# Kernel tuning notes

Hardware: AMD Instinct MI355X
Metric: run time of the kernel (lower is better)

## Reference

```python
import jax, jax.numpy as jnp
import numpy as np

N_TV_ITER = 20      # fixed Chambolle iteration count (skimage early-stops via eps; fixed for jit)
TV_WEIGHT = 0.1


def _div(p):
    # negative adjoint of forward-difference gradient (skimage convention)
    d = -(p[0] + p[1])
    d = d.at[1:, :].add(p[0, :-1, :])
    d = d.at[:, 1:].add(p[1, :, :-1])
    return d


def tv_chambolle_2d(image):
    """skimage.restoration.denoise_tv_chambolle on a single 2D image, weight=0.1."""
    tau = 0.25  # 1 / (2 * ndim)

    def step(p, _):
        out = image + _div(p)
        gy = jnp.zeros_like(out).at[:-1, :].set(out[1:, :] - out[:-1, :])
        gx = jnp.zeros_like(out).at[:, :-1].set(out[:, 1:] - out[:, :-1])
        norm = jnp.sqrt(gy * gy + gx * gx)
        g = jnp.stack([gy, gx])
        p = (p - tau * g) / (1.0 + (tau / TV_WEIGHT) * norm)
        return p, None

    p0 = jnp.zeros((2,) + image.shape, image.dtype)
    p, _ = jax.lax.scan(step, p0, None, length=N_TV_ITER)
    return image + _div(p)


def tv_denoise(img):  # [B,C,H,W], vmapped over B*C (replaces the CPU python loop)
    B, C, H, W = img.shape
    out = jax.vmap(tv_chambolle_2d)(img.reshape(B * C, H, W))
    return out.reshape(B, C, H, W)


def conv(x, w, stride=1, groups=1):
    pad = w.shape[2] // 2  # 'same'-style padding for odd kernels, 0 for 1x1
    return jax.lax.conv_general_dilated(
        x, w, (stride, stride), [(pad, pad), (pad, pad)],
        dimension_numbers=('NCHW', 'OIHW', 'NCHW'),
        feature_group_count=groups)


def haar_ll(x):
    # one level of pywt wavedec2('haar') LL band: 0.5 * sum over each 2x2 block
    return 0.5 * (x[..., ::2, ::2] + x[..., ::2, 1::2] + x[..., 1::2, ::2] + x[..., 1::2, 1::2])


def backbone(x, stem_w, dw_pw):
    # stride-32, 1280-channel EfficientNet-B0-style feature extractor
    x = jax.nn.silu(conv(x, stem_w, stride=2))
    for dw, pw in dw_pw:
        x = jax.nn.silu(conv(x, dw, stride=2, groups=dw.shape[0]))
        x = jax.nn.silu(conv(x, pw))
    return x


def setup_inputs() -> dict:
    key = jax.random.key(0)
    ks = jax.random.split(key, 16)
    B, H, W = 4, 512, 512

    def w(k, o, i, kh, kw):
        return jax.random.normal(k, (o, i, kh, kw), jnp.float32) * (1.0 / np.sqrt(i * kh * kw))

    return {
        "img": jax.random.normal(ks[0], (B, 1, H, W), jnp.float32),
        "stem_w": w(ks[1], 32, 1, 3, 3),
        "dw1_w": w(ks[2], 32, 1, 3, 3),  "pw1_w": w(ks[3], 64, 32, 1, 1),
        "dw2_w": w(ks[4], 64, 1, 3, 3),  "pw2_w": w(ks[5], 128, 64, 1, 1),
        "dw3_w": w(ks[6], 128, 1, 3, 3), "pw3_w": w(ks[7], 256, 128, 1, 1),
        "dw4_w": w(ks[8], 256, 1, 3, 3), "pw4_w": w(ks[9], 512, 256, 1, 1),
        "head_w": w(ks[10], 1280, 512, 1, 1),
        "proj_w": w(ks[11], 64, 1280, 1, 1),
        "proj_b": jnp.zeros((64,), jnp.float32),
        "final_w": w(ks[12], 1, 64, 1, 1),
        "final_b": jnp.zeros((1,), jnp.float32),
    }


def reference(img, stem_w, dw1_w, pw1_w, dw2_w, pw2_w, dw3_w, pw3_w, dw4_w, pw4_w,
              head_w, proj_w, proj_b, final_w, final_b):
    B, C, H, W = img.shape
    x = tv_denoise(img)                                     # fused TV Chambolle
    x = backbone(x, stem_w, [(dw1_w, pw1_w), (dw2_w, pw2_w), (dw3_w, pw3_w), (dw4_w, pw4_w)])
    x = jax.nn.silu(conv(x, head_w))                        # [B,1280,H/32,W/32]
    x = conv(x, proj_w) + proj_b[None, :, None, None]       # [B,64,H/32,W/32]
    x = jax.image.resize(x, (B, 64, H, W), method='bilinear')  # align_corners=False semantics
    ll = haar_ll(haar_ll(x))                                # 2-level Haar LL: [B,64,H/4,W/4]
    out = conv(ll, final_w) + final_b[None, :, None, None]  # [B,1,H/4,W/4]
    return out
```

## Files before the change

### kernel.cpp

```cpp
#include <hip/hip_runtime.h>
#include <math.h>

constexpr int BATCH = 4;
constexpr int IMG_H = 512, IMG_W = 512;
constexpr int IMG_HW = IMG_H * IMG_W;
constexpr int PSTR = BATCH * IMG_HW;

constexpr size_t O_PA   = 0;
constexpr size_t O_PB   = O_PA + 2 * (size_t)PSTR;
constexpr size_t O_DEN  = O_PB + 2 * (size_t)PSTR;
constexpr size_t O_A1   = O_DEN + (size_t)PSTR;
constexpr size_t O_A2   = O_A1 + 8388608;
constexpr size_t O_WT1  = O_A2 + 2097152;
constexpr size_t O_WT2  = O_WT1 + 32 * 64;
constexpr size_t O_WT3  = O_WT2 + 64 * 128;
constexpr size_t O_WT4  = O_WT3 + 128 * 256;
constexpr size_t O_WTH  = O_WT4 + 256 * 512;
constexpr size_t O_WCOMB= O_WTH + 512 * 1280;
constexpr size_t O_BCOMB= O_WCOMB + 1280;
constexpr size_t O_S    = O_BCOMB + 4;
constexpr size_t WS_FLOATS = O_S + 1024;

__device__ __forceinline__ float fast_rcp(float x) { return __builtin_amdgcn_rcpf(x); }
__device__ __forceinline__ float fast_sqrt(float x) { return __builtin_amdgcn_sqrtf(x); }
__device__ __forceinline__ float silu_f(float x) {
    float e = __builtin_amdgcn_exp2f(-1.44269504088896f * x);
    return x * fast_rcp(1.0f + e);
}
__device__ __forceinline__ int clampi(int v, int lo, int hi) {
    return v < lo ? lo : (v > hi ? hi : v);
}

template <int NST, bool FIRST, bool LAST>
__global__ __launch_bounds__(512, 8) void tv_reg(const float* __restrict__ img,
                                                 const float* __restrict__ pin,
                                                 float* __restrict__ pout,
                                                 const float* __restrict__ pw1,
                                                 const float* __restrict__ pw2,
                                                 const float* __restrict__ pw3,
                                                 const float* __restrict__ pw4,
                                                 const float* __restrict__ headw,
                                                 const float* __restrict__ projw,
                                                 const float* __restrict__ projb,
                                                 const float* __restrict__ finalw,
                                                 float* __restrict__ ws) {
    constexpr int ROWS = 6, NW = 8, HL = 10, TC = 44, TR = 28;
    constexpr int TVY = 19;
    __shared__ float bndP[2][512], bndO[2][512];

    if constexpr (FIRST) {
        if (blockIdx.y >= TVY) {
            __shared__ float tt[32][33];
            const int tid = threadIdx.x;
            const int pid = ((blockIdx.y - TVY) * 4 + blockIdx.z) * 12 + blockIdx.x;
            for (int t = pid; t < 814; t += 96) {
                const float* src = nullptr; float* dst = nullptr;
                int C = 0, R = 0, tr = 0, tc = 0;
                if (t < 640) {
                    src = headw; dst = ws + O_WTH; R = 1280; C = 512; tr = t >> 4; tc = t & 15;
                } else if (t < 768) {
                    int e = t - 640; src = pw4; dst = ws + O_WT4; R = 512; C = 256; tr = e >> 3; tc = e & 7;
                } else if (t < 800) {
                    int e = t - 768; src = pw3; dst = ws + O_WT3; R = 256; C = 128; tr = e >> 2; tc = e & 3;
                } else if (t < 808) {
                    int e = t - 800; src = pw2; dst = ws + O_WT2; R = 128; C = 64; tr = e >> 1; tc = e & 1;
                } else if (t < 810) {
                    int e = t - 808; src = pw1; dst = ws + O_WT1; R = 64; C = 32; tr = e; tc = 0;
                }
                const int tx = tid & 31, ty = tid >> 5;
                __syncthreads();
                if (src) {
#pragma unroll
                    for (int j = 0; j < 2; ++j)
                        tt[ty + j * 16][tx] =
                            src[(size_t)(tr * 32 + ty + j * 16) * C + tc * 32 + tx];
                }
                __syncthreads();
                if (src) {
#pragma unroll
                    for (int j = 0; j < 2; ++j)
                        dst[(size_t)(tc * 32 + ty + j * 16) * R + tr * 32 + tx] =
                            tt[tx][ty + j * 16];
                } else if (t < 813) {
                    int k = (t - 810) * 512 + tid;
                    if (k < 1280) {
                        float a = 0.0f;
                        for (int ch = 0; ch < 64; ++ch)
                            a = fmaf(finalw[ch], projw[ch * 1280 + k], a);
                        ws[O_WCOMB + k] = a;
                    }
                } else {
                    if (tid == 0) {
                        float a = 0.0f;
                        for (int ch = 0; ch < 64; ++ch) a = fmaf(finalw[ch], projb[ch], a);
                        ws[O_BCOMB] = a;
                    }
                }
            }
            return;
        }
    }

    const int tid = threadIdx.x;
    const int lane = tid & 63, w = tid >> 6;
    const int b = blockIdx.z;
    const int r0 = blockIdx.y * TR, c0 = blockIdx.x * TC;
    const int gj = c0 - HL + lane;
    const int gjc = clampi(gj, 0, 511);
    const int gib = r0 - HL + w * ROWS;
    const float* I = img + b * IMG_HW;
    const bool interior = (r0 - HL >= 1) && (r0 + NW * ROWS - HL <= 511) &&
                          (c0 - HL >= 1) && (c0 + 64 - HL <= 511);

    float rim[ROWS], rp0[ROWS], rp1[ROWS], ro[ROWS];
#pragma unroll
    for (int k = 0; k < ROWS; ++k) {
        int gi = clampi(gib + k, 0, 511);
        rim[k] = I[(gi << 9) + gjc];
    }
    if (!FIRST) {
        const float* P0 = pin + b * IMG_HW;
        const float* P1 = pin + PSTR + b * IMG_HW;
#pragma unroll
        for (int k = 0; k < ROWS; ++k) {
            int gi = clampi(gib + k, 0, 511);
            rp0[k] = P0[(gi << 9) + gjc];
            rp1[k] = P1[(gi << 9) + gjc];
        }
    }
    const bool gjpos = (gj > 0), gjlt = (gj < 511);

    int s0 = 0;
    if (FIRST) {
        bndO[0][tid] = rim[0];
        __syncthreads();
        float odn = (w < NW - 1) ? bndO[0][tid + 64] : 0.0f;
        if (interior) {
#pragma unroll
            for (int k = 0; k < ROWS; ++k) {
                float oR = __shfl_down(rim[k], 1);
                float od = (k < ROWS - 1) ? rim[k + 1] : odn;
                float gy = od - rim[k];
                float gx = oR - rim[k];
                float inv = fast_rcp(fmaf(2.5f, fast_sqrt(fmaf(gy, gy, gx * gx)), 1.0f));
                rp0[k] = -0.25f * gy * inv;
                rp1[k] = -0.25f * gx * inv;
            }
        } else {
#pragma unroll
            for (int k = 0; k < ROWS; ++k) {
                float oR = __shfl_down(rim[k], 1);
                float od = (k < ROWS - 1) ? rim[k + 1] : odn;
                int gi = gib + k;
                float gy = (gi < 511) ? od - rim[k] : 0.0f;
                float gx = gjlt ? oR - rim[k] : 0.0f;
                float inv = fast_rcp(fmaf(2.5f, fast_sqrt(fmaf(gy, gy, gx * gx)), 1.0f));
                rp0[k] = -0.25f * gy * inv;
                rp1[k] = -0.25f * gx * inv;
            }
        }
        s0 = 1;
    }

    for (int s = s0; s < NST; ++s) {
        const int par = s & 1;
        float p1l0 = __shfl_up(rp1[0], 1);
        float partO = rim[0] - rp0[0] - rp1[0];
        if (interior) partO += p1l0;
        else if (gjpos) partO += p1l0;
        bndP[par][tid] = rp0[ROWS - 1];
        bndO[par][tid] = partO;
        __syncthreads();
        float pup0 = (w > 0) ? bndP[par][tid - 64] : 0.0f;
        float odn = (w < NW - 1) ? bndO[par][tid + 64] + rp0[ROWS - 1] : 0.0f;
        if (interior) {
            ro[0] = partO + pup0;
#pragma unroll
            for (int k = 1; k < ROWS; ++k) {
                float p1l = __shfl_up(rp1[k], 1);
                ro[k] = rim[k] - rp0[k] - rp1[k] + rp0[k - 1] + p1l;
            }
#pragma unroll
            for (int k = 0; k < ROWS; ++k) {
                float oR = __shfl_down(ro[k], 1);
                float od = (k < ROWS - 1) ? ro[k + 1] : odn;
                float gy = od - ro[k];
                float gx = oR - ro[k];
                float inv = fast_rcp(fmaf(2.5f, fast_sqrt(fmaf(gy, gy, gx * gx)), 1.0f));
                rp0[k] = (rp0[k] - 0.25f * gy) * inv;
                rp1[k] = (rp1[k] - 0.25f * gx) * inv;
            }
        } else {
            ro[0] = partO + ((gib > 0) ? pup0 : 0.0f);
#pragma unroll
            for (int k = 1; k < ROWS; ++k) {
                float p1l = __shfl_up(rp1[k], 1);
                float o = rim[k] - rp0[k] - rp1[k];
                if (gib + k > 0) o += rp0[k - 1];
                if (gjpos) o += p1l;
                ro[k] = o;
            }
#pragma unroll
            for (int k = 0; k < ROWS; ++k) {
                float oR = __shfl_down(ro[k], 1);
                float od = (k < ROWS - 1) ? ro[k + 1] : odn;
                int gi = gib + k;
                float gy = (gi < 511) ? od - ro[k] : 0.0f;
                float gx = gjlt ? oR - ro[k] : 0.0f;
                float inv = fast_rcp(fmaf(2.5f, fast_sqrt(fmaf(gy, gy, gx * gx)), 1.0f));
                rp0[k] = (rp0[k] - 0.25f * gy) * inv;
                rp1[k] = (rp1[k] - 0.25f * gx) * inv;
            }
        }
    }

    const bool cst = (lane >= HL && lane < HL + TC && gj < 512);
    if (LAST) {
        constexpr int epar = NST & 1;
        bndP[epar][tid] = rp0[ROWS - 1];
        __syncthreads();
        float pup0 = (w > 0) ? bndP[epar][tid - 64] : 0.0f;
        float* D = pout + b * IMG_HW;
#pragma unroll
        for (int k = 0; k < ROWS; ++k) {
            float p1l = __shfl_up(rp1[k], 1);
            int gi = gib + k;
            int rk = w * ROWS + k;
            float o = rim[k] - rp0[k] - rp1[k];
            float pup = (k > 0) ? rp0[k - 1] : pup0;
            if (gi > 0) o += pup;
            if (gjpos) o += p1l;
            if (rk >= HL && rk < HL + TR && cst && gi < 512) D[(gi << 9) + gj] = o;
        }
    } else {
        float* Q0 = pout + b * IMG_HW;
        float* Q1 = pout + PSTR + b * IMG_HW;
#pragma unroll
        for (int k = 0; k < ROWS; ++k) {
            int rk = w * ROWS + k;
            int gi = gib + k;
            if (rk >= HL && rk < HL + TR && cst && gi < 512) {
                Q0[(gi << 9) + gj] = rp0[k];
                Q1[(gi << 9) + gj] = rp1[k];
            }
        }
    }
}

__global__ __launch_bounds__(256) void stem_dw1_pw1(const float* __restrict__ den,
                                                    const float* __restrict__ stemw,
                                                    const float* __restrict__ dw1w,
                                                    const float* __restrict__ pw1T,
                                                    float* __restrict__ out) {
    __shared__ float sDen[35 * 36];
    __shared__ float sStem[8 * 323];
    __shared__ float sDw[32 * 64];
    __shared__ float sW[576];
    __shared__ __align__(16) float sWp[2048];
    const int tid = threadIdx.x;
    const int b = blockIdx.z;
    const int r0 = blockIdx.y * 32, c0 = blockIdx.x * 32;
    const float* D = den + b * IMG_HW;
    for (int e = tid; e < 576; e += 256) sW[e] = (e < 288) ? stemw[e] : dw1w[e - 288];
    for (int e = tid; e < 2048; e += 256) sWp[e] = pw1T[e];
    for (int e = tid; e < 35 * 35; e += 256) {
        int li = e / 35, lj = e % 35;
        int gi = r0 - 3 + li, gjj = c0 - 3 + lj;
        sDen[li * 36 + lj] = (gi >= 0 && gjj >= 0) ? D[(gi << 9) + gjj] : 0.0f;
    }
    __syncthreads();

    for (int g = 0; g < 4; ++g) {
        if (g) __syncthreads();
        for (int e = tid; e < 2312; e += 256) {
            int pos = e >> 3, cl = e & 7;
            int sy = pos / 17, sx = pos % 17;
            int c = 8 * g + cl;
            const float* wc = &sW[c * 9];
            const float* dbase = &sDen[(2 * sy) * 36 + 2 * sx];
            float a = 0.0f;
#pragma unroll
            for (int ky = 0; ky < 3; ++ky)
#pragma unroll
                for (int kx = 0; kx < 3; ++kx)
                    a = fmaf(wc[ky * 3 + kx], dbase[ky * 36 + kx], a);
            sStem[cl * 323 + sy * 19 + sx] = silu_f(a);
        }
        __syncthreads();
        for (int e = tid; e < 512; e += 256) {
            int cl = e >> 6, dy = (e >> 3) & 7, dx = e & 7;
            int c = 8 * g + cl;
            float acc = 0.0f;
#pragma unroll
            for (int ky = 0; ky < 3; ++ky)
#pragma unroll
                for (int kx = 0; kx < 3; ++kx) {
                    int sgy = (r0 >> 1) - 1 + 2 * dy + ky;
                    int sgx = (c0 >> 1) - 1 + 2 * dx + kx;
                    float v = (sgy >= 0 && sgx >= 0)
                        ? sStem[cl * 323 + (2 * dy + ky) * 19 + 2 * dx + kx] : 0.0f;
                    acc = fmaf(sW[288 + c * 9 + ky * 3 + kx], v, acc);
                }
            sDw[c * 64 + (dy << 3) + dx] = silu_f(acc);
        }
    }
    __syncthreads();

    const int px = tid & 63, oc0 = (tid >> 6) * 16;
    float acc[16];
#pragma unroll
    for (int j = 0; j < 16; ++j) acc[j] = 0.0f;
    for (int ic = 0; ic < 32; ++ic) {
        float v = sDw[ic * 64 + px];
        const float* wr = &sWp[ic * 64 + oc0];
#pragma unroll
        for (int q = 0; q < 4; ++q) {
            float4 w4 = *(const float4*)(wr + q * 4);
            acc[q * 4 + 0] = fmaf(v, w4.x, acc[q * 4 + 0]);
            acc[q * 4 + 1] = fmaf(v, w4.y, acc[q * 4 + 1]);
            acc[q * 4 + 2] = fmaf(v, w4.z, acc[q * 4 + 2]);
            acc[q * 4 + 3] = fmaf(v, w4.w, acc[q * 4 + 3]);
        }
    }
    const int gpos = ((r0 >> 2) + (px >> 3)) * 128 + (c0 >> 2) + (px & 7);
    float* ob = out + (size_t)b * 64 * 16384 + (size_t)oc0 * 16384 + gpos;
#pragma unroll
    for (int j = 0; j < 16; ++j) ob[(size_t)j * 16384] = silu_f(acc[j]);
}

template <int C, int HIN>
__global__ __launch_bounds__(256) void dw_kernel(const float* __restrict__ in,
                                                 const float* __restrict__ w,
                                                 float* __restrict__ out) {
    constexpr int HO = HIN / 2;
    int t = blockIdx.x * 256 + threadIdx.x;
    int x = t % HO;
    int y = (t / HO) % HO;
    int c = (t / (HO * HO)) % C;
    int b = t / (HO * HO * C);
    const float* I = in + ((size_t)(b * C + c)) * (HIN * HIN);
    const float* wc = w + c * 9;
    int iy = 2 * y - 1, ix = 2 * x - 1;
    float acc = 0.0f;
#pragma unroll
    for (int ky = 0; ky < 3; ++ky)
#pragma unroll
        for (int kx = 0; kx < 3; ++kx) {
            int yy = iy + ky, xx = ix + kx;
            float vv = (yy >= 0 && xx >= 0) ? I[yy * HIN + xx] : 0.0f;
            acc = fmaf(wc[ky * 3 + kx], vv, acc);
        }
    out[t] = silu_f(acc);
}

template <int C, int HIN>
__global__ __launch_bounds__(256) void dw_reduce2_kernel(const float* __restrict__ part,
                                                         const float* __restrict__ w,
                                                         float* __restrict__ out) {
    constexpr int HO = HIN / 2;
    int t = blockIdx.x * 256 + threadIdx.x;
    int x = t % HO;
    int y = (t / HO) % HO;
    int c = (t / (HO * HO)) % C;
    int b = t / (HO * HO * C);
    const float* Ia = part + ((size_t)(b * C + c)) * (HIN * HIN);
    const float* Ib = Ia + (size_t)BATCH * C * HIN * HIN;
    const float* wc = w + c * 9;
    int iy = 2 * y - 1, ix = 2 * x - 1;
    float acc = 0.0f;
#pragma unroll
    for (int ky = 0; ky < 3; ++ky)
#pragma unroll
        for (int kx = 0; kx < 3; ++kx) {
            int yy = iy + ky, xx = ix + kx;
            float vv = 0.0f;
            if (yy >= 0 && xx >= 0) {
                int o = yy * HIN + xx;
                vv = silu_f(Ia[o] + Ib[o]);
            }
            acc = fmaf(wc[ky * 3 + kx], vv, acc);
        }
    out[t] = silu_f(acc);
}

template <int ICT, int NSIN, int NSPLIT, int OC, bool SILU>
__global__ __launch_bounds__(256) void pw_gemm(const float* __restrict__ in,
                                               const float* __restrict__ wT,
                                               float* __restrict__ out,
                                               int HW) {
    constexpr int KC = 32, TP = 64, TOC = 64, OPT = 4, PPT = 4;
    constexpr int KS = ICT / NSPLIT;
    constexpr int NC = KS / KC;
    constexpr int NOG = TOC / OPT;
    constexpr int PV4 = KC * TP / 4 / 256;
    constexpr int WV4 = KC * TOC / 4 / 256;
    static_assert(KS % KC == 0, "split");
    __shared__ __align__(16) float sPx[2][KC * TP];
    __shared__ __align__(16) float sW[2][KC * TOC];
    const int tid = threadIdx.x;
    const int zb = blockIdx.z;
    const int b = zb / NSPLIT, ks = zb % NSPLIT;
    const int p0 = blockIdx.x * TP;
    const int oc0 = blockIdx.y * TOC;
    const int ocg = tid % NOG, pxg = tid / NOG;
    const size_t instride = (size_t)BATCH * ICT * HW;
    const float* gin0 = in + ((size_t)b * ICT + ks * KS) * HW + p0;
    const float* gw0  = wT + ((size_t)(ks * KS)) * OC + oc0;

    float4 rp[PV4], rw[WV4];
    auto load_chunk = [&](int cc) {
        const float* gin = gin0 + (size_t)cc * KC * HW;
#pragma unroll
        for (int i = 0; i < PV4; ++i) {
            int e = tid + i * 256;
            int row = e / (TP / 4), col = e % (TP / 4);
            const float* base = gin + (size_t)row * HW + col * 4;
            float4 a = *(const float4*)base;
#pragma unroll
            for (int s = 1; s < NSIN; ++s) {
                float4 t4 = *(const float4*)(base + (size_t)s * instride);
                a.x += t4.x; a.y += t4.y; a.z += t4.z; a.w += t4.w;
            }
            if (NSIN > 1) {
                a.x = silu_f(a.x); a.y = silu_f(a.y);
                a.z = silu_f(a.z); a.w = silu_f(a.w);
            }
            rp[i] = a;
        }
        const float* gw = gw0 + (size_t)cc * KC * OC;
#pragma unroll
        for (int i = 0; i < WV4; ++i) {
            int e = tid + i * 256;
            int row = e / (TOC / 4), col = e % (TOC / 4);
            rw[i] = *(const float4*)(gw + (size_t)row * OC + col * 4);
        }
    };
    auto store_chunk = [&](int buf) {
#pragma unroll
        for (int i = 0; i < PV4; ++i) ((float4*)sPx[buf])[tid + i * 256] = rp[i];
#pragma unroll
        for (int i = 0; i < WV4; ++i) ((float4*)sW[buf])[tid + i * 256] = rw[i];
    };

    float acc[OPT][PPT];
#pragma unroll
    for (int o = 0; o < OPT; ++o)
#pragma unroll
        for (int p = 0; p < PPT; ++p) acc[o][p] = 0.0f;

    load_chunk(0);
    store_chunk(0);
    __syncthreads();
    for (int cc = 0; cc < NC; ++cc) {
        if (cc + 1 < NC) load_chunk(cc + 1);
        const int buf = cc & 1;
#pragma unroll 4
        for (int k = 0; k < KC; ++k) {
            float4 pv = *(const float4*)&sPx[buf][k * TP + pxg * PPT];
            float4 wv = *(const float4*)&sW[buf][k * TOC + ocg * OPT];
            float w0 = wv.x, w1 = wv.y, w2 = wv.z, w3 = wv.w;
            acc[0][0] = fmaf(pv.x, w0, acc[0][0]);
            acc[0][1] = fmaf(pv.y, w0, acc[0][1]);
            acc[0][2] = fmaf(pv.z, w0, acc[0][2]);
            acc[0][3] = fmaf(pv.w, w0, acc[0][3]);
            acc[1][0] = fmaf(pv.x, w1, acc[1][0]);
            acc[1][1] = fmaf(pv.y, w1, acc[1][1]);
            acc[1][2] = fmaf(pv.z, w1, acc[1][2]);
            acc[1][3] = fmaf(pv.w, w1, acc[1][3]);
            acc[2][0] = fmaf(pv.x, w2, acc[2][0]);
            acc[2][1] = fmaf(pv.y, w2, acc[2][1]);
            acc[2][2] = fmaf(pv.z, w2, acc[2][2]);
            acc[2][3] = fmaf(pv.w, w2, acc[2][3]);
            acc[3][0] = fmaf(pv.x, w3, acc[3][0]);
            acc[3][1] = fmaf(pv.y, w3, acc[3][1]);
            acc[3][2] = fmaf(pv.z, w3, acc[3][2]);
            acc[3][3] = fmaf(pv.w, w3, acc[3][3]);
        }
        if (cc + 1 < NC) {
            store_chunk((cc + 1) & 1);
            __syncthreads();
        }
    }

    float* ob;
    if (NSPLIT == 1)
        ob = out + ((size_t)(b * OC + oc0 + ocg * OPT)) * HW + p0 + pxg * PPT;
    else
        ob = out + (((size_t)(ks * BATCH + b)) * OC + oc0 + ocg * OPT) * HW + p0 + pxg * PPT;
#pragma unroll
    for (int o = 0; o < OPT; ++o) {
        float4 r;
        r.x = SILU ? silu_f(acc[o][0]) : acc[o][0];
        r.y = SILU ? silu_f(acc[o][1]) : acc[o][1];
        r.z = SILU ? silu_f(acc[o][2]) : acc[o][2];
        r.w = SILU ? silu_f(acc[o][3]) : acc[o][3];
        *(float4*)(ob + (size_t)o * HW) = r;
    }
}

__global__ __launch_bounds__(256) void presum_silu(const float* __restrict__ part,
                                                   float* __restrict__ xout) {
    constexpr size_t PS = (size_t)BATCH * 512 * 256;
    int t = blockIdx.x * 256 + threadIdx.x;
    const float* p = part + (size_t)t * 4;
    float4 a = *(const float4*)p;
    float4 b = *(const float4*)(p + PS);
    float4 c = *(const float4*)(p + 2 * PS);
    float4 d = *(const float4*)(p + 3 * PS);
    a.x += b.x; a.y += b.y; a.z += b.z; a.w += b.w;
    a.x += c.x; a.y += c.y; a.z += c.z; a.w += c.w;
    a.x += d.x; a.y += d.y; a.z += d.z; a.w += d.w;
    a.x = silu_f(a.x); a.y = silu_f(a.y); a.z = silu_f(a.z); a.w = silu_f(a.w);
    *(float4*)(xout + (size_t)t * 4) = a;
}

__global__ __launch_bounds__(256) void head_fused(const float* __restrict__ x,
                                                  const float* __restrict__ wT,
                                                  const float* __restrict__ wcomb,
                                                  float* __restrict__ partial) {
    constexpr int KC = 32, TP = 64, OC = 1280, HW = 256, NC = 16;
    __shared__ __align__(16) float sPx[2][KC * TP];
    __shared__ float dotred[64 * 16];
    const int tid = threadIdx.x;
    const int b = blockIdx.z;
    const int p0 = blockIdx.x * TP;
    const int oc0 = blockIdx.y * 128;
    const int ocg = tid & 15, pxg = tid >> 4;
    const float* gin0 = x + (size_t)b * 512 * HW + p0;
    const float* gw0 = wT + oc0 + ocg * 8;

    float4 rp[2];
    auto load_px = [&](int cc) {
        const float* gin = gin0 + (size_t)cc * KC * HW;
#pragma unroll
        for (int i = 0; i < 2; ++i) {
            int e = tid + i * 256;
            int row = e >> 4, col = e & 15;
            rp[i] = *(const float4*)(gin + (size_t)row * HW + col * 4);
        }
    };
    auto store_px = [&](int buf) {
#pragma unroll
        for (int i = 0; i < 2; ++i) ((float4*)sPx[buf])[tid + i * 256] = rp[i];
    };

    float acc[8][4];
#pragma unroll
    for (int o = 0; o < 8; ++o)
#pragma unroll
        for (int p = 0; p < 4; ++p) acc[o][p] = 0.0f;

    load_px(0);
    store_px(0);
    __syncthreads();
    for (int cc = 0; cc < NC; ++cc) {
        if (cc + 1 < NC) load_px(cc + 1);
        const float* sp = sPx[cc & 1];
        const float* gw = gw0 + (size_t)cc * KC * OC;
#pragma unroll 8
        for (int k = 0; k < KC; ++k) {
            float4 w0 = *(const float4*)(gw + (size_t)k * OC);
            float4 w1 = *(const float4*)(gw + (size_t)k * OC + 4);
            float4 pv = *(const float4*)&sp[k * TP + pxg * 4];
            acc[0][0] = fmaf(pv.x, w0.x, acc[0][0]);
            acc[0][1] = fmaf(pv.y, w0.x, acc[0][1]);
            acc[0][2] = fmaf(pv.z, w0.x, acc[0][2]);
            acc[0][3] = fmaf(pv.w, w0.x, acc[0][3]);
            acc[1][0] = fmaf(pv.x, w0.y, acc[1][0]);
            acc[1][1] = fmaf(pv.y, w0.y, acc[1][1]);
            acc[1][2] = fmaf(pv.z, w0.y, acc[1][2]);
            acc[1][3] = fmaf(pv.w, w0.y, acc[1][3]);
            acc[2][0] = fmaf(pv.x, w0.z, acc[2][0]);
            acc[2][1] = fmaf(pv.y, w0.z, acc[2][1]);
            acc[2][2] = fmaf(pv.z, w0.z, acc[2][2]);
            acc[2][3] = fmaf(pv.w, w0.z, acc[2][3]);
            acc[3][0] = fmaf(pv.x, w0.w, acc[3][0]);
            acc[3][1] = fmaf(pv.y, w0.w, acc[3][1]);
            acc[3][2] = fmaf(pv.z, w0.w, acc[3][2]);
            acc[3][3] = fmaf(pv.w, w0.w, acc[3][3]);
            acc[4][0] = fmaf(pv.x, w1.x, acc[4][0]);
            acc[4][1] = fmaf(pv.y, w1.x, acc[4][1]);
            acc[4][2] = fmaf(pv.z, w1.x, acc[4][2]);
            acc[4][3] = fmaf(pv.w, w1.x, acc[4][3]);
            acc[5][0] = fmaf(pv.x, w1.y, acc[5][0]);
            acc[5][1] = fmaf(pv.y, w1.y, acc[5][1]);
            acc[5][2] = fmaf(pv.z, w1.y, acc[5][2]);
            acc[5][3] = fmaf(pv.w, w1.y, acc[5][3]);
            acc[6][0] = fmaf(pv.x, w1.z, acc[6][0]);
            acc[6][1] = fmaf(pv.y, w1.z, acc[6][1]);
            acc[6][2] = fmaf(pv.z, w1.z, acc[6][2]);
            acc[6][3] = fmaf(pv.w, w1.z, acc[6][3]);
            acc[7][0] = fmaf(pv.x, w1.w, acc[7][0]);
            acc[7][1] = fmaf(pv.y, w1.w, acc[7][1]);
            acc[7][2] = fmaf(pv.z, w1.w, acc[7][2]);
            acc[7][3] = fmaf(pv.w, w1.w, acc[7][3]);
        }
        if (cc + 1 < NC) {
            store_px((cc + 1) & 1);
            __syncthreads();
        }
    }

    float4 wcA = *(const float4*)(wcomb + oc0 + ocg * 8);
    float4 wcB = *(const float4*)(wcomb + oc0 + ocg * 8 + 4);
#pragma unroll
    for (int p = 0; p < 4; ++p) {
        float v = wcA.x * silu_f(acc[0][p]);
        v = fmaf(wcA.y, silu_f(acc[1][p]), v);
        v = fmaf(wcA.z, silu_f(acc[2][p]), v);
        v = fmaf(wcA.w, silu_f(acc[3][p]), v);
        v = fmaf(wcB.x, silu_f(acc[4][p]), v);
        v = fmaf(wcB.y, silu_f(acc[5][p]), v);
        v = fmaf(wcB.z, silu_f(acc[6][p]), v);
        v = fmaf(wcB.w, silu_f(acc[7][p]), v);
        dotred[(pxg * 4 + p) * 16 + ocg] = v;
    }
    __syncthreads();
    if (tid < 64) {
        float a = 0.0f;
#pragma unroll
        for (int gg = 0; gg < 16; ++gg) a += dotred[tid * 16 + gg];
        partial[((size_t)blockIdx.y * 4 + b) * 256 + p0 + tid] = a;
    }
}

__global__ __launch_bounds__(256) void resize_haar(const float* __restrict__ partial,
                                                   const float* __restrict__ bcomb,
                                                   const float* __restrict__ finalb,
                                                   float* __restrict__ out) {
    __shared__ float sS[256];
    int t = blockIdx.x * 256 + threadIdx.x;
    int c = t & 127, r = (t >> 7) & 127, b = t >> 14;
    {
        float a = bcomb[0];
        const float* P = partial + (size_t)b * 256 + threadIdx.x;
        for (int y = 0; y < 10; ++y) a += P[(size_t)y * 1024];
        sS[threadIdx.x] = a;
    }
    __syncthreads();
    const float* S = sS;
    float acc = 0.0f;
#pragma unroll
    for (int j = 0; j < 4; ++j) {
        float sy = ((4 * r + j) + 0.5f) * (1.0f / 32.0f) - 0.5f;
        int y0 = (int)floorf(sy);
        float fy = sy - (float)y0;
        int ya = y0 < 0 ? 0 : y0;
        int yb = (y0 + 1) > 15 ? 15 : (y0 + 1);
#pragma unroll
        for (int i = 0; i < 4; ++i) {
            float sx = ((4 * c + i) + 0.5f) * (1.0f / 32.0f) - 0.5f;
            int x0 = (int)floorf(sx);
            float fx = sx - (float)x0;
            int xa = x0 < 0 ? 0 : x0;
            int xb = (x0 + 1) > 15 ? 15 : (x0 + 1);
            float v0 = S[ya * 16 + xa] * (1.0f - fx) + S[ya * 16 + xb] * fx;
            float v1 = S[yb * 16 + xa] * (1.0f - fx) + S[yb * 16 + xb] * fx;
            acc += v0 * (1.0f - fy) + v1 * fy;
        }
    }
    out[t] = 0.25f * acc + finalb[0];
}

extern "C" void kernel_launch(void* const* d_in, const int* in_sizes, int n_in,
                              void* d_out, int out_size, void* d_ws, size_t ws_size,
                              hipStream_t stream) {
    if (ws_size < WS_FLOATS * sizeof(float)) return;

    const float* img    = (const float*)d_in[0];
    const float* stem_w = (const float*)d_in[1];
    const float* dw1_w  = (const float*)d_in[2];
    const float* pw1_w  = (const float*)d_in[3];
    const float* dw2_w  = (const float*)d_in[4];
    const float* pw2_w  = (const float*)d_in[5];
    const float* dw3_w  = (const float*)d_in[6];
    const float* pw3_w  = (const float*)d_in[7];
    const float* dw4_w  = (const float*)d_in[8];
    const float* pw4_w  = (const float*)d_in[9];
    const float* head_w = (const float*)d_in[10];
    const float* proj_w = (const float*)d_in[11];
    const float* proj_b = (const float*)d_in[12];
    const float* final_w= (const float*)d_in[13];
    const float* final_b= (const float*)d_in[14];
    float* ws  = (float*)d_ws;
    float* out = (float*)d_out;

    dim3 tvg1(12, 21, 4), tvg2(12, 19, 4);
    tv_reg<10, true,  false><<<tvg1, 512, 0, stream>>>(
        img, img, ws + O_PA,
        pw1_w, pw2_w, pw3_w, pw4_w, head_w, proj_w, proj_b, final_w, ws);
    tv_reg<10, false, true ><<<tvg2, 512, 0, stream>>>(
        img, ws + O_PA, ws + O_DEN,
        nullptr, nullptr, nullptr, nullptr, nullptr, nullptr, nullptr, nullptr, ws);

    stem_dw1_pw1<<<dim3(16, 16, 4), 256, 0, stream>>>(ws + O_DEN, stem_w, dw1_w,
                                                      ws + O_WT1, ws + O_A1);

    dw_kernel<64, 128><<<4096, 256, 0, stream>>>(ws + O_A1, dw2_w, ws + O_A2);
    pw_gemm<64, 1, 2, 128, false><<<dim3(64, 2, 8), 256, 0, stream>>>(ws + O_A2, ws + O_WT2, ws + O_PA, 4096);

    dw_reduce2_kernel<128, 64><<<2048, 256, 0, stream>>>(ws + O_PA, dw3_w, ws + O_A1);
    pw_gemm<128, 1, 2, 256, false><<<dim3(16, 4, 8), 256, 0, stream>>>(ws + O_A1, ws + O_WT3, ws + O_PA, 1024);

    dw_reduce2_kernel<256, 32><<<1024, 256, 0, stream>>>(ws + O_PA, dw4_w, ws + O_A2);
    pw_gemm<256, 1, 4, 512, false><<<dim3(4, 8, 16), 256, 0, stream>>>(ws + O_A2, ws + O_WT4, ws + O_PA, 256);

    presum_silu<<<512, 256, 0, stream>>>(ws + O_PA, ws + O_A2);

    head_fused<<<dim3(4, 10, 4), 256, 0, stream>>>(ws + O_A2, ws + O_WTH, ws + O_WCOMB, ws + O_A1);

    resize_haar<<<256, 256, 0, stream>>>(ws + O_A1, ws + O_BCOMB, final_b, out);
}
```

Before: 293.8 us.

## Retile head GEMM with split-K warps and LDS-staged weights for more blocks

The head 1x1 conv kernel now uses smaller tiles (32 pixels x 64 output channels) with 128 threads. The two 64-thread groups each handle half of the 512 input channels and combine their partial sums through shared memory. Weights are now staged in LDS with double buffering instead of being read straight from global memory per k. The grid grows from 160 to 640 blocks to fill more CUs, so resize_haar now sums 20 partials instead of 10. The cost is more shared memory per block and an extra reduction step.

```diff
diff --git a/kernel.cpp b/kernel.cpp
--- a/kernel.cpp
+++ b/kernel.cpp
@@ -514,34 +514,49 @@
     *(float4*)(xout + (size_t)t * 4) = a;
 }
 
-__global__ __launch_bounds__(256) void head_fused(const float* __restrict__ x,
+__global__ __launch_bounds__(128) void head_fused(const float* __restrict__ x,
                                                   const float* __restrict__ wT,
                                                   const float* __restrict__ wcomb,
                                                   float* __restrict__ partial) {
-    constexpr int KC = 32, TP = 64, OC = 1280, HW = 256, NC = 16;
-    __shared__ __align__(16) float sPx[2][KC * TP];
-    __shared__ float dotred[64 * 16];
+    constexpr int KC = 32, TP = 32, TOC = 64, OC = 1280, HW = 256;
+    constexpr int NCG = 8;
+    __shared__ __align__(16) float smem[4096 + 8192 + 256];
+    float* pxBuf = smem;
+    float* wBuf  = smem + 4096;
+    float* dotred= smem + 12288;
+    float* kred  = smem;
     const int tid = threadIdx.x;
+    const int g = tid >> 6, lane = tid & 63;
     const int b = blockIdx.z;
     const int p0 = blockIdx.x * TP;
-    const int oc0 = blockIdx.y * 128;
-    const int ocg = tid & 15, pxg = tid >> 4;
+    const int oc0 = blockIdx.y * TOC;
+    const int ocg = lane & 7, pxg = lane >> 3;
     const float* gin0 = x + (size_t)b * 512 * HW + p0;
-    const float* gw0 = wT + oc0 + ocg * 8;
-
-    float4 rp[2];
-    auto load_px = [&](int cc) {
-        const float* gin = gin0 + (size_t)cc * KC * HW;
-#pragma unroll
-        for (int i = 0; i < 2; ++i) {
-            int e = tid + i * 256;
+
+    float4 rp[4], rw[8];
+    auto load_chunk = [&](int cc) {
+        const float* gin = gin0 + (size_t)(g * NCG + cc) * KC * HW;
+#pragma unroll
+        for (int i = 0; i < 4; ++i) {
+            int e = lane + i * 64;
+            int row = e >> 3, col = e & 7;
+            rp[i] = *(const float4*)(gin + (size_t)row * HW + col * 4);
+        }
+        const float* gw = wT + (size_t)(g * NCG + cc) * KC * OC + oc0;
+#pragma unroll
+        for (int i = 0; i < 8; ++i) {
+            int e = lane + i * 64;
             int row = e >> 4, col = e & 15;
-            rp[i] = *(const float4*)(gin + (size_t)row * HW + col * 4);
+            rw[i] = *(const float4*)(gw + (size_t)row * OC + col * 4);
         }
     };
-    auto store_px = [&](int buf) {
-#pragma unroll
-        for (int i = 0; i < 2; ++i) ((float4*)sPx[buf])[tid + i * 256] = rp[i];
+    auto store_chunk = [&](int buf) {
+        float4* sp = (float4*)(pxBuf + (g * 2 + buf) * 1024);
+        float4* sw = (float4*)(wBuf + (g * 2 + buf) * 2048);
+#pragma unroll
+        for (int i = 0; i < 4; ++i) sp[lane + i * 64] = rp[i];
+#pragma unroll
+        for (int i = 0; i < 8; ++i) sw[lane + i * 64] = rw[i];
     };
 
     float acc[8][4];
@@ -550,18 +565,18 @@
 #pragma unroll
         for (int p = 0; p < 4; ++p) acc[o][p] = 0.0f;
 
-    load_px(0);
-    store_px(0);
+    load_chunk(0);
+    store_chunk(0);
     __syncthreads();
-    for (int cc = 0; cc < NC; ++cc) {
-        if (cc + 1 < NC) load_px(cc + 1);
-        const float* sp = sPx[cc & 1];
-        const float* gw = gw0 + (size_t)cc * KC * OC;
-#pragma unroll 8
+    for (int cc = 0; cc < NCG; ++cc) {
+        if (cc + 1 < NCG) load_chunk(cc + 1);
+        const float* sp = pxBuf + (g * 2 + (cc & 1)) * 1024;
+        const float* sw = wBuf + (g * 2 + (cc & 1)) * 2048;
+#pragma unroll 4
         for (int k = 0; k < KC; ++k) {
-            float4 w0 = *(const float4*)(gw + (size_t)k * OC);
-            float4 w1 = *(const float4*)(gw + (size_t)k * OC + 4);
             float4 pv = *(const float4*)&sp[k * TP + pxg * 4];
+            float4 w0 = *(const float4*)&sw[k * TOC + ocg * 8];
+            float4 w1 = *(const float4*)&sw[k * TOC + ocg * 8 + 4];
             acc[0][0] = fmaf(pv.x, w0.x, acc[0][0]);
             acc[0][1] = fmaf(pv.y, w0.x, acc[0][1]);
             acc[0][2] = fmaf(pv.z, w0.x, acc[0][2]);
@@ -595,31 +610,45 @@
             acc[7][2] = fmaf(pv.z, w1.w, acc[7][2]);
             acc[7][3] = fmaf(pv.w, w1.w, acc[7][3]);
         }
-        if (cc + 1 < NC) {
-            store_px((cc + 1) & 1);
+        if (cc + 1 < NCG) {
+            store_chunk((cc + 1) & 1);
             __syncthreads();
         }
     }
 
-    float4 wcA = *(const float4*)(wcomb + oc0 + ocg * 8);
-    float4 wcB = *(const float4*)(wcomb + oc0 + ocg * 8 + 4);
-#pragma unroll
-    for (int p = 0; p < 4; ++p) {
-        float v = wcA.x * silu_f(acc[0][p]);
-        v = fmaf(wcA.y, silu_f(acc[1][p]), v);
-        v = fmaf(wcA.z, silu_f(acc[2][p]), v);
-        v = fmaf(wcA.w, silu_f(acc[3][p]), v);
-        v = fmaf(wcB.x, silu_f(acc[4][p]), v);
-        v = fmaf(wcB.y, silu_f(acc[5][p]), v);
-        v = fmaf(wcB.z, silu_f(acc[6][p]), v);
-        v = fmaf(wcB.w, silu_f(acc[7][p]), v);
-        dotred[(pxg * 4 + p) * 16 + ocg] = v;
-    }
     __syncthreads();
-    if (tid < 64) {
+    if (g == 1) {
+#pragma unroll
+        for (int o = 0; o < 8; ++o)
+#pragma unroll
+            for (int p = 0; p < 4; ++p) kred[lane * 32 + o * 4 + p] = acc[o][p];
+    }
+    __syncthreads();
+    if (g == 0) {
+#pragma unroll
+        for (int o = 0; o < 8; ++o)
+#pragma unroll
+            for (int p = 0; p < 4; ++p) acc[o][p] += kred[lane * 32 + o * 4 + p];
+        float4 wcA = *(const float4*)(wcomb + oc0 + ocg * 8);
+        float4 wcB = *(const float4*)(wcomb + oc0 + ocg * 8 + 4);
+#pragma unroll
+        for (int p = 0; p < 4; ++p) {
+            float v = wcA.x * silu_f(acc[0][p]);
+            v = fmaf(wcA.y, silu_f(acc[1][p]), v);
+            v = fmaf(wcA.z, silu_f(acc[2][p]), v);
+            v = fmaf(wcA.w, silu_f(acc[3][p]), v);
+            v = fmaf(wcB.x, silu_f(acc[4][p]), v);
+            v = fmaf(wcB.y, silu_f(acc[5][p]), v);
+            v = fmaf(wcB.z, silu_f(acc[6][p]), v);
+            v = fmaf(wcB.w, silu_f(acc[7][p]), v);
+            dotred[(pxg * 4 + p) * 8 + ocg] = v;
+        }
+    }
+    __syncthreads();
+    if (tid < 32) {
         float a = 0.0f;
 #pragma unroll
-        for (int gg = 0; gg < 16; ++gg) a += dotred[tid * 16 + gg];
+        for (int gg = 0; gg < 8; ++gg) a += dotred[tid * 8 + gg];
         partial[((size_t)blockIdx.y * 4 + b) * 256 + p0 + tid] = a;
     }
 }
@@ -634,7 +663,7 @@
     {
         float a = bcomb[0];
         const float* P = partial + (size_t)b * 256 + threadIdx.x;
-        for (int y = 0; y < 10; ++y) a += P[(size_t)y * 1024];
+        for (int y = 0; y < 20; ++y) a += P[(size_t)y * 1024];
         sS[threadIdx.x] = a;
     }
     __syncthreads();
@@ -707,7 +736,7 @@
 
     presum_silu<<<512, 256, 0, stream>>>(ws + O_PA, ws + O_A2);
 
-    head_fused<<<dim3(4, 10, 4), 256, 0, stream>>>(ws + O_A2, ws + O_WTH, ws + O_WCOMB, ws + O_A1);
+    head_fused<<<dim3(8, 20, 4), 128, 0, stream>>>(ws + O_A2, ws + O_WTH, ws + O_WCOMB, ws + O_A1);
 
     resize_haar<<<256, 256, 0, stream>>>(ws + O_A1, ws + O_BCOMB, final_b, out);
 }
```

New measurement: 251.8 us. 14.3% less time.
